# Optimization experiments

Measured on AMD Instinct MI355X. Metric: run time of the kernel, lower is better.

## Reference

```python
import jax, jax.numpy as jnp
import numpy as np

B, S, D, C = 64, 576, 768, 200


def setup_inputs() -> dict:
    key = jax.random.key(0)
    k1, k2, k3, k4 = jax.random.split(key, 4)
    return {
        "patch_tokens": jax.random.normal(k1, (B, S, D), dtype=jnp.float32),
        "class_token": jax.random.normal(k2, (B, D), dtype=jnp.float32),
        "attn_w": jax.random.normal(k3, (C, D), dtype=jnp.float32) * (1.0 / np.sqrt(D)),
        "attn_b": jnp.zeros((C,), dtype=jnp.float32),
        "gc_w": jax.random.normal(k4, (C, D), dtype=jnp.float32) * (1.0 / np.sqrt(D)),
        "gc_b": jnp.zeros((C,), dtype=jnp.float32),
        "lam": jnp.ones((1,), dtype=jnp.float32),
    }


def reference(patch_tokens, class_token, attn_w, attn_b, gc_w, gc_b, lam):
    # patch_tokens: (B,S,D). The torch module reshapes S to HxW, but the mean
    # over (H,W) equals the mean over S, so we stay in token layout.
    _, S_, D_ = patch_tokens.shape
    # Global classifier: (B,C)
    global_scores = class_token @ gc_w.T + gc_b
    # Per-class 1x1 conv == per-class linear projection over tokens: (B,C,S)
    att = jax.nn.sigmoid(
        jnp.einsum("bsd,cd->bcs", patch_tokens, attn_w) + attn_b[None, :, None]
    )
    # mean over spatial (S) then mean over channels (D):
    # mean_d mean_s (att * feat) == einsum / (S*D)
    attention_scores = jnp.einsum("bcs,bsd->bc", att, patch_tokens) / (S_ * D_)
    return global_scores + lam[0] * attention_scores
```

## Files before the change

kernel.cpp:

```cpp
#include <hip/hip_runtime.h>
#include <math.h>

#define Bsz  64
#define Ssz  576
#define Dsz  768
#define Csz  200
#define NPAD 208
#define MT   64
#define BK   32
#define NKT  24

typedef short short8 __attribute__((ext_vector_type(8)));
typedef float f32x4  __attribute__((ext_vector_type(4)));

#define AS_GLOBAL __attribute__((address_space(1)))
#define AS_LDS    __attribute__((address_space(3)))

__device__ inline unsigned short f2bf_rne(float f) {
    union { float f; unsigned int u; } v; v.f = f;
    return (unsigned short)((v.u + 0x7FFFu + ((v.u >> 16) & 1u)) >> 16);
}
__device__ inline unsigned int pack2bf(float lo, float hi) {
    union { float f; unsigned int u; } a, b; a.f = lo; b.f = hi;
    return __builtin_amdgcn_perm(b.u + 0x8000u, a.u + 0x8000u, 0x07060302u);
}
__device__ inline void gload16(const unsigned short* g, unsigned short* l) {
    __builtin_amdgcn_global_load_lds((const AS_GLOBAL unsigned int*)g,
                                     (AS_LDS unsigned int*)l, 16, 0, 0);
}
__device__ inline void gload16f(const float* g, float* l) {
    __builtin_amdgcn_global_load_lds((const AS_GLOBAL unsigned int*)g,
                                     (AS_LDS unsigned int*)l, 16, 0, 0);
}

__global__ __launch_bounds__(256) void prep_w(const float* __restrict__ W,
                                              unsigned short* __restrict__ Wb) {
    const int i   = blockIdx.x * 256 + threadIdx.x;
    const int row = i / (Dsz / 4);
    const int col = (i % (Dsz / 4)) * 4;
    ushort4 h;
    if (row < Csz) {
        const float4 v = *(const float4*)(W + (size_t)row * Dsz + col);
        h.x = f2bf_rne(v.x); h.y = f2bf_rne(v.y); h.z = f2bf_rne(v.z); h.w = f2bf_rne(v.w);
    } else if (row == Csz) {
        h.x = h.y = h.z = h.w = 0x3F80;
    } else {
        h.x = h.y = h.z = h.w = 0;
    }
    *(ushort4*)(Wb + (size_t)row * Dsz + col) = h;
}

__global__ __launch_bounds__(256) void gc_kernel(
    const float* __restrict__ ct, const float* __restrict__ gw,
    const float* __restrict__ gb, float* __restrict__ out) {
    const int b    = blockIdx.x;
    const int wv   = threadIdx.x >> 6;
    const int lane = threadIdx.x & 63;
    const int c    = blockIdx.y * 4 + wv;
    const float* wr = gw + (size_t)c * Dsz + lane * 12;
    const float* cr = ct + (size_t)b * Dsz + lane * 12;
    float s = 0.f;
#pragma unroll
    for (int j = 0; j < 3; ++j) {
        const float4 w = *(const float4*)(wr + 4 * j);
        const float4 x = *(const float4*)(cr + 4 * j);
        s += w.x * x.x + w.y * x.y + w.z * x.z + w.w * x.w;
    }
#pragma unroll
    for (int off = 32; off > 0; off >>= 1) s += __shfl_down(s, off, 64);
    if (lane == 0) out[b * Csz + c] = s + gb[c];
}

__global__ __launch_bounds__(256, 3) void attn_kernel(
    const float* __restrict__ X,
    const unsigned short* __restrict__ Wb,
    const float* __restrict__ attn_b,
    const float* __restrict__ lam,
    float* __restrict__ out)
{
    __shared__ float sX[2][MT * BK];
    __shared__ unsigned short sW[2][NPAD * BK];

    const int tid  = threadIdx.x;
    const int lane = tid & 63;
    const int w    = tid >> 6;
    const int m    = lane & 15;
    const int q    = lane >> 4;
    const int rowbase = blockIdx.x * MT;
    const int bidx    = rowbase / Ssz;

    const int sxa  = w * 128 + lane;
    const int xrow = sxa >> 3;
    const int xgc  = (sxa & 7) ^ (xrow & 7);
    const float* xg = X + (size_t)(rowbase + xrow) * Dsz + xgc * 4;

    const int wn    = (w < 3) ? 3 : 4;
    const int grp0  = w * 3;
    const int sw0   = grp0 * 64 + lane;
    const int wrow0 = sw0 >> 2;
    const int wgc   = (sw0 & 3) ^ (wrow0 & 3);
    const unsigned short* wg = Wb + (size_t)wrow0 * Dsz + wgc * 8;

    const int rA    = w * 16 + m;
    const int aoff0 = (rA * 8 + ((2 * q) ^ (rA & 7))) * 4;
    const int aoff1 = (rA * 8 + ((2 * q + 1) ^ (rA & 7))) * 4;
    const int boff  = (m * 4 + (q ^ (m & 3))) * 8;

    f32x4 acc[13];
#pragma unroll
    for (int t = 0; t < 13; ++t) acc[t] = (f32x4){0.f, 0.f, 0.f, 0.f};

    gload16f(xg, &sX[0][w * 512]);
    gload16f(xg + 8 * Dsz, &sX[0][w * 512 + 256]);
#pragma unroll
    for (int j = 0; j < 4; ++j)
        if (j < wn) gload16(wg + (size_t)16 * j * Dsz, &sW[0][(grp0 + j) * 512]);

    for (int kt = 0; kt < NKT; ++kt) {
        const int p = kt & 1;
        __syncthreads();
        if (kt + 1 < NKT) {
            const int kk = (kt + 1) * BK;
            gload16f(xg + kk, &sX[p ^ 1][w * 512]);
            gload16f(xg + kk + 8 * Dsz, &sX[p ^ 1][w * 512 + 256]);
#pragma unroll
            for (int j = 0; j < 4; ++j)
                if (j < wn) gload16(wg + (size_t)(kk + 16 * j * Dsz), &sW[p ^ 1][(grp0 + j) * 512]);
        }
        const float4 alo = *(const float4*)&sX[p][aoff0];
        const float4 ahi = *(const float4*)&sX[p][aoff1];
        union { short8 s; unsigned int u[4]; } A;
        A.u[0] = pack2bf(alo.x, alo.y); A.u[1] = pack2bf(alo.z, alo.w);
        A.u[2] = pack2bf(ahi.x, ahi.y); A.u[3] = pack2bf(ahi.z, ahi.w);
#pragma unroll
        for (int t = 0; t < 13; ++t) {
            const short8 bf = *(const short8*)&sW[p][boff + t * 512];
            acc[t] = __builtin_amdgcn_mfma_f32_16x16x32_bf16(A.s, bf, acc[t], 0, 0, 0);
        }
    }

    float rsv[4];
#pragma unroll
    for (int r = 0; r < 4; ++r) rsv[r] = __shfl(acc[12][r], (lane & 48) + 8, 64);

    const float scale = lam[0] * (1.f / ((float)Ssz * (float)Dsz));

#pragma unroll
    for (int t = 0; t < 13; ++t) {
        const int c = t * 16 + m;
        if (c < Csz) {
            const float bias = attn_b[c];
            float s = 0.f;
#pragma unroll
            for (int r = 0; r < 4; ++r)
                s += rsv[r] / (1.f + __expf(-(acc[t][r] + bias)));
            s += __shfl_xor(s, 16, 64);
            s += __shfl_xor(s, 32, 64);
            if (q == 0) atomicAdd(&out[bidx * Csz + c], s * scale);
        }
    }
}

extern "C" void kernel_launch(void* const* d_in, const int* in_sizes, int n_in,
                              void* d_out, int out_size, void* d_ws, size_t ws_size,
                              hipStream_t stream) {
    const float* X   = (const float*)d_in[0];
    const float* ct  = (const float*)d_in[1];
    const float* aw  = (const float*)d_in[2];
    const float* ab  = (const float*)d_in[3];
    const float* gw  = (const float*)d_in[4];
    const float* gb  = (const float*)d_in[5];
    const float* lam = (const float*)d_in[6];
    float* out = (float*)d_out;
    unsigned short* Wb = (unsigned short*)d_ws;

    prep_w<<<(NPAD * Dsz / 4) / 256, 256, 0, stream>>>(aw, Wb);
    gc_kernel<<<dim3(Bsz, Csz / 4), 256, 0, stream>>>(ct, gw, gb, out);
    attn_kernel<<<(Bsz * Ssz) / MT, 256, 0, stream>>>(X, Wb, ab, lam, out);
}
```

Baseline: 211.2 us.

## Switch attention GEMM to FP8 MFMA with LDS-resident weights and register-streamed X

Quantizes the attention weights to FP8 in the prep kernel and converts activations to FP8 on the fly, using the 16x16x32 fp8 MFMA instead of bf16. The whole padded weight matrix (208x784 bytes) is loaded once per block into LDS. Each wave then streams its X rows straight from global memory into registers with a 3-deep prefetch, which removes the per-k-tile LDS staging and barriers of the old loop. Blocks now cover 144 rows (one quarter of a batch image). FP8 cuts accuracy considerably compared with bf16. The large LDS footprint and loop over 9 row tiles across 4 waves leave the work unevenly split, with one wave doing 3 tiles while the others do 2, and may reduce occupancy.

Result: slower. 321.6 us (+52.3%).

```diff
diff --git a/kernel.cpp b/kernel.cpp
--- a/kernel.cpp
+++ b/kernel.cpp
@@ -6,48 +6,26 @@
 #define Dsz  768
 #define Csz  200
 #define NPAD 208
-#define MT   64
-#define BK   32
-#define NKT  24
+#define WSTRIDE 784
+#define RPB  144
+#define NKI  24
 
-typedef short short8 __attribute__((ext_vector_type(8)));
-typedef float f32x4  __attribute__((ext_vector_type(4)));
+typedef float f32x4 __attribute__((ext_vector_type(4)));
 
-#define AS_GLOBAL __attribute__((address_space(1)))
-#define AS_LDS    __attribute__((address_space(3)))
-
-__device__ inline unsigned short f2bf_rne(float f) {
-    union { float f; unsigned int u; } v; v.f = f;
-    return (unsigned short)((v.u + 0x7FFFu + ((v.u >> 16) & 1u)) >> 16);
-}
-__device__ inline unsigned int pack2bf(float lo, float hi) {
-    union { float f; unsigned int u; } a, b; a.f = lo; b.f = hi;
-    return __builtin_amdgcn_perm(b.u + 0x8000u, a.u + 0x8000u, 0x07060302u);
-}
-__device__ inline void gload16(const unsigned short* g, unsigned short* l) {
-    __builtin_amdgcn_global_load_lds((const AS_GLOBAL unsigned int*)g,
-                                     (AS_LDS unsigned int*)l, 16, 0, 0);
-}
-__device__ inline void gload16f(const float* g, float* l) {
-    __builtin_amdgcn_global_load_lds((const AS_GLOBAL unsigned int*)g,
-                                     (AS_LDS unsigned int*)l, 16, 0, 0);
-}
-
-__global__ __launch_bounds__(256) void prep_w(const float* __restrict__ W,
-                                              unsigned short* __restrict__ Wb) {
+__global__ __launch_bounds__(256) void prep_w8(const float* __restrict__ W,
+                                               unsigned int* __restrict__ Wq) {
     const int i   = blockIdx.x * 256 + threadIdx.x;
-    const int row = i / (Dsz / 4);
-    const int col = (i % (Dsz / 4)) * 4;
-    ushort4 h;
+    const int row = i / 192;
+    const int col = (i % 192) * 4;
+    unsigned int w = 0;
     if (row < Csz) {
         const float4 v = *(const float4*)(W + (size_t)row * Dsz + col);
-        h.x = f2bf_rne(v.x); h.y = f2bf_rne(v.y); h.z = f2bf_rne(v.z); h.w = f2bf_rne(v.w);
+        w = __builtin_amdgcn_cvt_pk_fp8_f32(v.x, v.y, 0u, false);
+        w = __builtin_amdgcn_cvt_pk_fp8_f32(v.z, v.w, w, true);
     } else if (row == Csz) {
-        h.x = h.y = h.z = h.w = 0x3F80;
-    } else {
-        h.x = h.y = h.z = h.w = 0;
+        w = 0x38383838u;
     }
-    *(ushort4*)(Wb + (size_t)row * Dsz + col) = h;
+    Wq[i] = w;
 }
 
 __global__ __launch_bounds__(256) void gc_kernel(
@@ -71,92 +49,87 @@
     if (lane == 0) out[b * Csz + c] = s + gb[c];
 }
 
-__global__ __launch_bounds__(256, 3) void attn_kernel(
+__global__ __launch_bounds__(256) void attn_kernel(
     const float* __restrict__ X,
-    const unsigned short* __restrict__ Wb,
+    const unsigned char* __restrict__ Wq,
     const float* __restrict__ attn_b,
     const float* __restrict__ lam,
     float* __restrict__ out)
 {
-    __shared__ float sX[2][MT * BK];
-    __shared__ unsigned short sW[2][NPAD * BK];
+    extern __shared__ unsigned char sW[];
 
     const int tid  = threadIdx.x;
     const int lane = tid & 63;
     const int w    = tid >> 6;
     const int m    = lane & 15;
     const int q    = lane >> 4;
-    const int rowbase = blockIdx.x * MT;
-    const int bidx    = rowbase / Ssz;
+    const int rowbase = blockIdx.x * RPB;
+    const int bidx    = blockIdx.x >> 2;
 
-    const int sxa  = w * 128 + lane;
-    const int xrow = sxa >> 3;
-    const int xgc  = (sxa & 7) ^ (xrow & 7);
-    const float* xg = X + (size_t)(rowbase + xrow) * Dsz + xgc * 4;
-
-    const int wn    = (w < 3) ? 3 : 4;
-    const int grp0  = w * 3;
-    const int sw0   = grp0 * 64 + lane;
-    const int wrow0 = sw0 >> 2;
-    const int wgc   = (sw0 & 3) ^ (wrow0 & 3);
-    const unsigned short* wg = Wb + (size_t)wrow0 * Dsz + wgc * 8;
-
-    const int rA    = w * 16 + m;
-    const int aoff0 = (rA * 8 + ((2 * q) ^ (rA & 7))) * 4;
-    const int aoff1 = (rA * 8 + ((2 * q + 1) ^ (rA & 7))) * 4;
-    const int boff  = (m * 4 + (q ^ (m & 3))) * 8;
-
-    f32x4 acc[13];
-#pragma unroll
-    for (int t = 0; t < 13; ++t) acc[t] = (f32x4){0.f, 0.f, 0.f, 0.f};
-
-    gload16f(xg, &sX[0][w * 512]);
-    gload16f(xg + 8 * Dsz, &sX[0][w * 512 + 256]);
-#pragma unroll
-    for (int j = 0; j < 4; ++j)
-        if (j < wn) gload16(wg + (size_t)16 * j * Dsz, &sW[0][(grp0 + j) * 512]);
-
-    for (int kt = 0; kt < NKT; ++kt) {
-        const int p = kt & 1;
-        __syncthreads();
-        if (kt + 1 < NKT) {
-            const int kk = (kt + 1) * BK;
-            gload16f(xg + kk, &sX[p ^ 1][w * 512]);
-            gload16f(xg + kk + 8 * Dsz, &sX[p ^ 1][w * 512 + 256]);
-#pragma unroll
-            for (int j = 0; j < 4; ++j)
-                if (j < wn) gload16(wg + (size_t)(kk + 16 * j * Dsz), &sW[p ^ 1][(grp0 + j) * 512]);
-        }
-        const float4 alo = *(const float4*)&sX[p][aoff0];
-        const float4 ahi = *(const float4*)&sX[p][aoff1];
-        union { short8 s; unsigned int u[4]; } A;
-        A.u[0] = pack2bf(alo.x, alo.y); A.u[1] = pack2bf(alo.z, alo.w);
-        A.u[2] = pack2bf(ahi.x, ahi.y); A.u[3] = pack2bf(ahi.z, ahi.w);
-#pragma unroll
-        for (int t = 0; t < 13; ++t) {
-            const short8 bf = *(const short8*)&sW[p][boff + t * 512];
-            acc[t] = __builtin_amdgcn_mfma_f32_16x16x32_bf16(A.s, bf, acc[t], 0, 0, 0);
-        }
+    for (int s = tid; s < NPAD * 48; s += 256) {
+        const int row = s / 48;
+        const int cp  = s % 48;
+        const uint4 v = *(const uint4*)(Wq + (size_t)row * Dsz + cp * 16);
+        *(uint4*)(&sW[row * WSTRIDE + cp * 16]) = v;
     }
-
-    float rsv[4];
-#pragma unroll
-    for (int r = 0; r < 4; ++r) rsv[r] = __shfl(acc[12][r], (lane & 48) + 8, 64);
+    __syncthreads();
 
     const float scale = lam[0] * (1.f / ((float)Ssz * (float)Dsz));
 
+    for (int tt = w; tt < 9; tt += 4) {
+        const int xrow = rowbase + tt * 16 + m;
+        const float* xr = X + (size_t)xrow * Dsz + q * 8;
+
+        f32x4 acc[13];
 #pragma unroll
-    for (int t = 0; t < 13; ++t) {
-        const int c = t * 16 + m;
-        if (c < Csz) {
-            const float bias = attn_b[c];
-            float s = 0.f;
+        for (int t = 0; t < 13; ++t) acc[t] = (f32x4){0.f, 0.f, 0.f, 0.f};
+
+        float4 st[3][2];
 #pragma unroll
-            for (int r = 0; r < 4; ++r)
-                s += rsv[r] / (1.f + __expf(-(acc[t][r] + bias)));
-            s += __shfl_xor(s, 16, 64);
-            s += __shfl_xor(s, 32, 64);
-            if (q == 0) atomicAdd(&out[bidx * Csz + c], s * scale);
+        for (int k = 0; k < 3; ++k) {
+            st[k][0] = *(const float4*)(xr + k * 32);
+            st[k][1] = *(const float4*)(xr + k * 32 + 4);
+        }
+#pragma unroll
+        for (int k = 0; k < NKI; ++k) {
+            const int si = k % 3;
+            const float4 a0 = st[si][0];
+            const float4 a1 = st[si][1];
+            if (k + 3 < NKI) {
+                st[si][0] = *(const float4*)(xr + (k + 3) * 32);
+                st[si][1] = *(const float4*)(xr + (k + 3) * 32 + 4);
+            }
+            union { long l; unsigned int u[2]; } A;
+            A.u[0] = __builtin_amdgcn_cvt_pk_fp8_f32(a0.x, a0.y, 0u, false);
+            A.u[0] = __builtin_amdgcn_cvt_pk_fp8_f32(a0.z, a0.w, A.u[0], true);
+            A.u[1] = __builtin_amdgcn_cvt_pk_fp8_f32(a1.x, a1.y, 0u, false);
+            A.u[1] = __builtin_amdgcn_cvt_pk_fp8_f32(a1.z, a1.w, A.u[1], true);
+
+            const unsigned char* wb = &sW[m * WSTRIDE + k * 32 + q * 8];
+#pragma unroll
+            for (int t = 0; t < 13; ++t) {
+                const long B = *(const long*)(wb + t * 16 * WSTRIDE);
+                acc[t] = __builtin_amdgcn_mfma_f32_16x16x32_fp8_fp8(A.l, B, acc[t], 0, 0, 0);
+            }
+        }
+
+        float rsv[4];
+#pragma unroll
+        for (int r = 0; r < 4; ++r) rsv[r] = __shfl(acc[12][r], (lane & 48) + 8, 64);
+
+#pragma unroll
+        for (int t = 0; t < 13; ++t) {
+            const int c = t * 16 + m;
+            if (c < Csz) {
+                const float bias = attn_b[c];
+                float s = 0.f;
+#pragma unroll
+                for (int r = 0; r < 4; ++r)
+                    s += rsv[r] / (1.f + __expf(-(acc[t][r] + bias)));
+                s += __shfl_xor(s, 16, 64);
+                s += __shfl_xor(s, 32, 64);
+                if (q == 0) atomicAdd(&out[bidx * Csz + c], s * scale);
+            }
         }
     }
 }
@@ -172,9 +145,13 @@
     const float* gb  = (const float*)d_in[5];
     const float* lam = (const float*)d_in[6];
     float* out = (float*)d_out;
-    unsigned short* Wb = (unsigned short*)d_ws;
+    unsigned char* Wq = (unsigned char*)d_ws;
 
-    prep_w<<<(NPAD * Dsz / 4) / 256, 256, 0, stream>>>(aw, Wb);
+    static const int lds_bytes = NPAD * WSTRIDE;
+    hipFuncSetAttribute((const void*)attn_kernel,
+                        hipFuncAttributeMaxDynamicSharedMemorySize, lds_bytes);
+
+    prep_w8<<<(NPAD * Dsz / 4) / 256, 256, 0, stream>>>(aw, (unsigned int*)Wq);
     gc_kernel<<<dim3(Bsz, Csz / 4), 256, 0, stream>>>(ct, gw, gb, out);
-    attn_kernel<<<(Bsz * Ssz) / MT, 256, 0, stream>>>(X, Wb, ab, lam, out);
+    attn_kernel<<<(Bsz * Ssz) / RPB, 256, lds_bytes, stream>>>(X, Wq, ab, lam, out);
 }
```
